# Kernel tuning notes

Hardware: AMD Instinct MI355X
Metric: run time of the kernel (lower is better)

## Reference

```python
import jax, jax.numpy as jnp
import numpy as np

W = H = 64
CONFIGS = [(1, 3), (2, 3), (3, 3)]  # (dilation, kernel_size)
OUT_PER_CFG = 32
IN_CH = 32


def build_mask():
    # One (W+1, H+1) mask per config, broadcast over (out, in) channels.
    masks = []
    for d, k in CONFIGS:
        m = np.zeros((W + 1, H + 1), dtype=np.float32)
        k1 = (k - 1) * (d - 1) + k  # effective dilated kernel extent
        s1 = (W - k1) // 2 + 1
        e1 = (W + k1) // 2 + 1
        s2 = (H - k1) // 2 + 1
        e2 = (H + k1) // 2 + 1
        m[s1:e1:d, s2:e2:d] = 1.0
        masks.append(np.broadcast_to(m, (OUT_PER_CFG, 1, W + 1, H + 1)))
    return jnp.asarray(np.concatenate(masks, axis=0))  # (96, 1, 65, 65)


def setup_inputs() -> dict:
    key = jax.random.key(0)
    k1, k2 = jax.random.split(key)
    x = jax.random.normal(k1, (16, IN_CH, W, H), dtype=jnp.float32)
    # small init so tanh does not saturate
    weight = jax.random.normal(k2, (OUT_PER_CFG * len(CONFIGS), IN_CH, W + 1, H + 1), dtype=jnp.float32) * 0.01
    mask = build_mask()
    gamma = jnp.ones((OUT_PER_CFG * len(CONFIGS),), dtype=jnp.float32)
    beta = jnp.zeros((OUT_PER_CFG * len(CONFIGS),), dtype=jnp.float32)
    return {"x": x, "weight": weight, "mask": mask, "gamma": gamma, "beta": beta}


def reference(x, weight, mask, gamma, beta):
    # circular pad: last dim by H//2 each side, dim -2 by W//2 each side
    xp = jnp.pad(x, ((0, 0), (0, 0), (W // 2, W // 2), (H // 2, H // 2)), mode="wrap")
    y = jax.lax.conv_general_dilated(
        xp, weight * mask,
        window_strides=(1, 1), padding="VALID",
        dimension_numbers=("NCHW", "OIHW", "NCHW"),
    )  # (B, 96, 64, 64)
    # BatchNorm2d in training mode: batch statistics over (N, H, W), eps=1e-5
    mean = jnp.mean(y, axis=(0, 2, 3))
    var = jnp.var(y, axis=(0, 2, 3))
    yn = (y - mean[None, :, None, None]) * jax.lax.rsqrt(var + 1e-5)[None, :, None, None]
    yn = yn * gamma[None, :, None, None] + beta[None, :, None, None]
    return jnp.tanh(yn)
```

## Files before the change

kernel.cpp:

```cpp
#include <hip/hip_runtime.h>
#include <math.h>

#define BATCH 16
#define CIN 32
#define COUT 96
#define WH 64
#define IMG (WH*WH)
#define NPIX (BATCH*IMG)
#define YELEMS (BATCH*COUT*IMG)
#define NPART 256
#define PWELEMS (3*9*32*32)
#define XTELEMS (BATCH*IMG*CIN)

typedef __attribute__((ext_vector_type(8))) short short8;
typedef __attribute__((ext_vector_type(4))) float floatx4;

__device__ __forceinline__ unsigned short f2bf(float f) {
    union { float f; unsigned u; } v; v.f = f;
    unsigned r = v.u + 0x7FFFu + ((v.u >> 16) & 1u);
    return (unsigned short)(r >> 16);
}
__device__ __forceinline__ float bf2f(unsigned short u) {
    union { unsigned u; float f; } v; v.u = (unsigned)u << 16; return v.f;
}

#define GLDS(src, dst) __builtin_amdgcn_global_load_lds( \
    (const __attribute__((address_space(1))) void*)(src), \
    (__attribute__((address_space(3))) void*)(dst), 16, 0, 0)

__device__ __forceinline__ float fast_tanh(float xv) {
    float e = __expf(2.0f * xv);
    return fmaf(-2.0f, __builtin_amdgcn_rcpf(e + 1.0f), 1.0f);
}

__global__ __launch_bounds__(256) void prep_kernel(
    const float* __restrict__ x, const float* __restrict__ w,
    unsigned short* __restrict__ xT, unsigned short* __restrict__ pw)
{
    int blk = blockIdx.x;
    if (blk < 256) {
        int t   = blk * 256 + threadIdx.x;
        int b   = t >> 12;
        int pix = t & 4095;
        const float* xb = x + (size_t)b * CIN * IMG + pix;
        unsigned packed[16];
#pragma unroll
        for (int c2 = 0; c2 < 16; c2++) {
            unsigned short lo = f2bf(xb[(size_t)(2 * c2) * IMG]);
            unsigned short hi = f2bf(xb[(size_t)(2 * c2 + 1) * IMG]);
            packed[c2] = (unsigned)lo | ((unsigned)hi << 16);
        }
        uint4* dst = (uint4*)(xT + (size_t)t * 32);
#pragma unroll
        for (int k = 0; k < 4; k++)
            dst[k] = make_uint4(packed[4 * k], packed[4 * k + 1],
                                packed[4 * k + 2], packed[4 * k + 3]);
    } else {
        int e = (blk - 256) * 256 + threadIdx.x;
        if (e >= PWELEMS) return;
        int cfg = e / (9 * 1024);
        int rem = e % (9 * 1024);
        int tap = rem >> 10;
        int oc  = (rem >> 5) & 31;
        int c   = rem & 31;
        int d   = cfg + 1;
        int du  = tap / 3, dv = tap % 3;
        size_t idx = (((size_t)(cfg * 32 + oc) * CIN + c) * 65 + (32 + (du - 1) * d)) * 65
                     + (32 + (dv - 1) * d);
        pw[e] = f2bf(w[idx]);
    }
}

__global__ __launch_bounds__(256, 3) void conv_stats_kernel(
    const unsigned short* __restrict__ xT, const unsigned short* __restrict__ pw,
    unsigned short* __restrict__ yb, float* __restrict__ psum, float* __restrict__ psq)
{
    int bid  = blockIdx.x;
    int rowg = bid & 15;
    int rest = bid >> 4;
    int cfg  = rest % 3;
    int b    = rest / 3;
    int d    = cfg + 1;
    int i0   = rowg * 4;

    int t    = threadIdx.x;
    int wv   = t >> 6;
    int lane = t & 63;
    int l15  = lane & 15;
    int quad = lane >> 4;

    __shared__ __align__(16) unsigned short tile[10 * 2048];
    __shared__ float red_s[4][32];
    __shared__ float red_q[4][32];

    const unsigned short* xTb = xT + (size_t)b * IMG * 32;
#pragma unroll
    for (int rr = 0; rr < 10; rr++) {
        int gi = (i0 - 3 + rr) & 63;
        GLDS(xTb + (size_t)gi * 2048 + t * 8, &tile[rr * 2048 + t * 8]);
    }

    const unsigned short* pwc = pw + (size_t)cfg * 9 * 32 * 32;
    short8 af[2][9];
#pragma unroll
    for (int h = 0; h < 2; h++)
#pragma unroll
        for (int tap = 0; tap < 9; tap++)
            af[h][tap] = *(const short8*)(pwc + ((tap * 32 + h * 16 + l15) * 32 + quad * 8));

    __syncthreads();

    float ss[2][4], qq[2][4];
#pragma unroll
    for (int h = 0; h < 2; h++)
#pragma unroll
        for (int r = 0; r < 4; r++) { ss[h][r] = 0.f; qq[h][r] = 0.f; }

    int row = i0 + wv;
    size_t ybase = ((size_t)b * COUT + cfg * 32) * IMG + (size_t)row * WH;

#pragma unroll 1
    for (int cg = 0; cg < 4; cg++) {
        floatx4 a0 = {0.f, 0.f, 0.f, 0.f};
        floatx4 a1 = {0.f, 0.f, 0.f, 0.f};
#pragma unroll
        for (int du = 0; du < 3; du++) {
            int rowloc = wv + 3 + (du - 1) * d;
            const unsigned short* rbase = &tile[rowloc * 2048 + quad * 8];
#pragma unroll
            for (int dv = 0; dv < 3; dv++) {
                int col = (cg * 16 + l15 + (dv - 1) * d) & 63;
                short8 bf = *(const short8*)(rbase + col * 32);
                a0 = __builtin_amdgcn_mfma_f32_16x16x32_bf16(af[0][du * 3 + dv], bf, a0, 0, 0, 0);
                a1 = __builtin_amdgcn_mfma_f32_16x16x32_bf16(af[1][du * 3 + dv], bf, a1, 0, 0, 0);
            }
        }
        int colg = cg * 16 + l15;
#pragma unroll
        for (int r = 0; r < 4; r++) {
            float v0 = a0[r], v1 = a1[r];
            int m0 = quad * 4 + r;
            yb[ybase + (size_t)m0 * IMG + colg]        = f2bf(v0);
            yb[ybase + (size_t)(16 + m0) * IMG + colg] = f2bf(v1);
            ss[0][r] += v0; qq[0][r] = fmaf(v0, v0, qq[0][r]);
            ss[1][r] += v1; qq[1][r] = fmaf(v1, v1, qq[1][r]);
        }
    }

#pragma unroll
    for (int h = 0; h < 2; h++)
#pragma unroll
        for (int r = 0; r < 4; r++) {
            float s = ss[h][r], q = qq[h][r];
            for (int m = 1; m < 16; m <<= 1) {
                s += __shfl_xor(s, m, 64);
                q += __shfl_xor(q, m, 64);
            }
            if (l15 == 0) {
                red_s[wv][h * 16 + quad * 4 + r] = s;
                red_q[wv][h * 16 + quad * 4 + r] = q;
            }
        }
    __syncthreads();
    if (t < 32) {
        float S = red_s[0][t] + red_s[1][t] + red_s[2][t] + red_s[3][t];
        psum[(size_t)(cfg * 32 + t) * NPART + b * 16 + rowg] = S;
    } else if (t < 64) {
        int o = t - 32;
        float Q = red_q[0][o] + red_q[1][o] + red_q[2][o] + red_q[3][o];
        psq[(size_t)(cfg * 32 + o) * NPART + b * 16 + rowg] = Q;
    }
}

__global__ __launch_bounds__(256) void bn_tanh_kernel(
    const unsigned short* __restrict__ yb, const float* __restrict__ psum,
    const float* __restrict__ psq, const float* __restrict__ gamma,
    const float* __restrict__ beta, float* __restrict__ out)
{
    __shared__ float part[8];
    __shared__ float sc[2];
    int t  = threadIdx.x;
    int ch = blockIdx.x % COUT;

    float s = psum[(size_t)ch * NPART + t];
    float q = psq[(size_t)ch * NPART + t];
    for (int m = 1; m < 64; m <<= 1) {
        s += __shfl_xor(s, m, 64);
        q += __shfl_xor(q, m, 64);
    }
    if ((t & 63) == 0) { part[t >> 6] = s; part[4 + (t >> 6)] = q; }
    __syncthreads();
    if (t == 0) {
        const float inv_n = 1.0f / (float)NPIX;
        float S = part[0] + part[1] + part[2] + part[3];
        float Q = part[4] + part[5] + part[6] + part[7];
        float mean = S * inv_n;
        float var  = Q * inv_n - mean * mean;
        float a    = gamma[ch] * rsqrtf(var + 1e-5f);
        sc[0] = a;
        sc[1] = beta[ch] - mean * a;
    }
    __syncthreads();

    float a = sc[0], bsh = sc[1];
    size_t base = (size_t)blockIdx.x * IMG;
#pragma unroll
    for (int k = 0; k < 2; k++) {
        size_t off = base + k * 2048 + t * 8;
        uint4 raw = *(const uint4*)(yb + off);
        const unsigned short* u = (const unsigned short*)&raw;
        float4 r0, r1;
        r0.x = fast_tanh(fmaf(bf2f(u[0]), a, bsh));
        r0.y = fast_tanh(fmaf(bf2f(u[1]), a, bsh));
        r0.z = fast_tanh(fmaf(bf2f(u[2]), a, bsh));
        r0.w = fast_tanh(fmaf(bf2f(u[3]), a, bsh));
        r1.x = fast_tanh(fmaf(bf2f(u[4]), a, bsh));
        r1.y = fast_tanh(fmaf(bf2f(u[5]), a, bsh));
        r1.z = fast_tanh(fmaf(bf2f(u[6]), a, bsh));
        r1.w = fast_tanh(fmaf(bf2f(u[7]), a, bsh));
        *(float4*)(out + off)     = r0;
        *(float4*)(out + off + 4) = r1;
    }
}

extern "C" void kernel_launch(void* const* d_in, const int* in_sizes, int n_in,
                              void* d_out, int out_size, void* d_ws, size_t ws_size,
                              hipStream_t stream) {
    const float* x     = (const float*)d_in[0];
    const float* w     = (const float*)d_in[1];
    const float* gamma = (const float*)d_in[3];
    const float* beta  = (const float*)d_in[4];
    float* out = (float*)d_out;

    unsigned short* xT = (unsigned short*)d_ws;
    unsigned short* pw = xT + XTELEMS;
    unsigned short* yb = pw + PWELEMS + 32;
    float* psum = (float*)(yb + YELEMS);
    float* psq  = psum + COUT * NPART;

    prep_kernel<<<256 + (PWELEMS + 255) / 256, 256, 0, stream>>>(x, w, xT, pw);
    conv_stats_kernel<<<768, 256, 0, stream>>>(xT, pw, yb, psum, psq);
    bn_tanh_kernel<<<BATCH * COUT, 256, 0, stream>>>(yb, psum, psq, gamma, beta, out);
}
```

Before: 118.0 us.

## Fuse prep, conv+stats and BN+tanh into one cooperative kernel

Merges the three launches into a single cooperative kernel that uses two grid-wide syncs: one after converting x and the weights to bf16, and one after writing the partial BN statistics. The conv results stay packed in registers, so the bf16 intermediate y never goes to global memory and the separate bn_tanh pass is removed. This saves launch overhead and a round trip of y through memory. In exchange it relies on all 768 blocks being co-resident (3 per CU by launch bounds), adds grid-sync cost, and stores output with 16-wide strided scalar writes instead of vectorised ones. It falls back to the old three-kernel path if the cooperative launch fails.

```diff
diff --git a/kernel.cpp b/kernel.cpp
--- a/kernel.cpp
+++ b/kernel.cpp
@@ -1,4 +1,5 @@
 #include <hip/hip_runtime.h>
+#include <hip/hip_cooperative_groups.h>
 #include <math.h>
 
 #define BATCH 16
@@ -12,6 +13,8 @@
 #define PWELEMS (3*9*32*32)
 #define XTELEMS (BATCH*IMG*CIN)
 
+namespace coopg = cooperative_groups;
+
 typedef __attribute__((ext_vector_type(8))) short short8;
 typedef __attribute__((ext_vector_type(4))) float floatx4;
 
@@ -31,6 +34,194 @@
 __device__ __forceinline__ float fast_tanh(float xv) {
     float e = __expf(2.0f * xv);
     return fmaf(-2.0f, __builtin_amdgcn_rcpf(e + 1.0f), 1.0f);
+}
+
+__global__ __launch_bounds__(256, 3) void fused_kernel(
+    const float* __restrict__ x, const float* __restrict__ w,
+    unsigned short* __restrict__ xT, unsigned short* __restrict__ pw,
+    float* __restrict__ psum, float* __restrict__ psq,
+    const float* __restrict__ gamma, const float* __restrict__ beta,
+    float* __restrict__ out)
+{
+    __shared__ __align__(16) unsigned short tile[10 * 2048];
+    __shared__ float red_s[4][32];
+    __shared__ float red_q[4][32];
+    __shared__ float sc_a[32];
+    __shared__ float sc_b[32];
+
+    int t   = threadIdx.x;
+    int gid = blockIdx.x * 256 + t;
+
+    if (gid < 2 * NPIX) {
+        int pt   = gid >> 1;
+        int half = gid & 1;
+        int b    = pt >> 12;
+        int pix  = pt & 4095;
+        const float* xb = x + ((size_t)b * CIN + half * 16) * IMG + pix;
+        unsigned packed[8];
+#pragma unroll
+        for (int c2 = 0; c2 < 8; c2++) {
+            unsigned short lo = f2bf(xb[(size_t)(2 * c2) * IMG]);
+            unsigned short hi = f2bf(xb[(size_t)(2 * c2 + 1) * IMG]);
+            packed[c2] = (unsigned)lo | ((unsigned)hi << 16);
+        }
+        uint4* dst = (uint4*)(xT + (size_t)pt * 32 + half * 16);
+        dst[0] = make_uint4(packed[0], packed[1], packed[2], packed[3]);
+        dst[1] = make_uint4(packed[4], packed[5], packed[6], packed[7]);
+    } else if (gid < 2 * NPIX + PWELEMS) {
+        int e   = gid - 2 * NPIX;
+        int cfg = e / (9 * 1024);
+        int rem = e % (9 * 1024);
+        int tap = rem >> 10;
+        int oc  = (rem >> 5) & 31;
+        int c   = rem & 31;
+        int dd  = cfg + 1;
+        int du  = tap / 3, dv = tap % 3;
+        size_t idx = (((size_t)(cfg * 32 + oc) * CIN + c) * 65 + (32 + (du - 1) * dd)) * 65
+                     + (32 + (dv - 1) * dd);
+        pw[e] = f2bf(w[idx]);
+    }
+    __threadfence();
+    coopg::this_grid().sync();
+
+    int bid  = blockIdx.x;
+    int rowg = bid & 15;
+    int rest = bid >> 4;
+    int cfg  = rest % 3;
+    int b    = rest / 3;
+    int d    = cfg + 1;
+    int i0   = rowg * 4;
+
+    int wv   = t >> 6;
+    int lane = t & 63;
+    int l15  = lane & 15;
+    int quad = lane >> 4;
+
+    const unsigned short* xTb = xT + (size_t)b * IMG * 32;
+#pragma unroll
+    for (int rr = 0; rr < 10; rr++) {
+        int gi = (i0 - 3 + rr) & 63;
+        GLDS(xTb + (size_t)gi * 2048 + t * 8, &tile[rr * 2048 + t * 8]);
+    }
+
+    const unsigned short* pwc = pw + (size_t)cfg * 9 * 32 * 32;
+    short8 af[2][9];
+#pragma unroll
+    for (int h = 0; h < 2; h++)
+#pragma unroll
+        for (int tap = 0; tap < 9; tap++)
+            af[h][tap] = *(const short8*)(pwc + ((tap * 32 + h * 16 + l15) * 32 + quad * 8));
+
+    __syncthreads();
+
+    float ss[2][4], qq[2][4];
+#pragma unroll
+    for (int h = 0; h < 2; h++)
+#pragma unroll
+        for (int r = 0; r < 4; r++) { ss[h][r] = 0.f; qq[h][r] = 0.f; }
+
+    unsigned ypk[2][4][2];
+    int row = i0 + wv;
+
+#pragma unroll
+    for (int cgi = 0; cgi < 4; cgi++) {
+        floatx4 a0 = {0.f, 0.f, 0.f, 0.f};
+        floatx4 a1 = {0.f, 0.f, 0.f, 0.f};
+#pragma unroll
+        for (int du = 0; du < 3; du++) {
+            int rowloc = wv + 3 + (du - 1) * d;
+            const unsigned short* rbase = &tile[rowloc * 2048 + quad * 8];
+#pragma unroll
+            for (int dv = 0; dv < 3; dv++) {
+                int col = (cgi * 16 + l15 + (dv - 1) * d) & 63;
+                short8 bf = *(const short8*)(rbase + col * 32);
+                a0 = __builtin_amdgcn_mfma_f32_16x16x32_bf16(af[0][du * 3 + dv], bf, a0, 0, 0, 0);
+                a1 = __builtin_amdgcn_mfma_f32_16x16x32_bf16(af[1][du * 3 + dv], bf, a1, 0, 0, 0);
+            }
+        }
+#pragma unroll
+        for (int r = 0; r < 4; r++) {
+            float v0 = a0[r], v1 = a1[r];
+            unsigned short h0 = f2bf(v0), h1 = f2bf(v1);
+            if (cgi & 1) {
+                ypk[0][r][cgi >> 1] |= (unsigned)h0 << 16;
+                ypk[1][r][cgi >> 1] |= (unsigned)h1 << 16;
+            } else {
+                ypk[0][r][cgi >> 1] = (unsigned)h0;
+                ypk[1][r][cgi >> 1] = (unsigned)h1;
+            }
+            ss[0][r] += v0; qq[0][r] = fmaf(v0, v0, qq[0][r]);
+            ss[1][r] += v1; qq[1][r] = fmaf(v1, v1, qq[1][r]);
+        }
+    }
+
+#pragma unroll
+    for (int h = 0; h < 2; h++)
+#pragma unroll
+        for (int r = 0; r < 4; r++) {
+            float s = ss[h][r], q = qq[h][r];
+            for (int m = 1; m < 16; m <<= 1) {
+                s += __shfl_xor(s, m, 64);
+                q += __shfl_xor(q, m, 64);
+            }
+            if (l15 == 0) {
+                red_s[wv][h * 16 + quad * 4 + r] = s;
+                red_q[wv][h * 16 + quad * 4 + r] = q;
+            }
+        }
+    __syncthreads();
+    if (t < 32) {
+        float S = red_s[0][t] + red_s[1][t] + red_s[2][t] + red_s[3][t];
+        psum[(size_t)(cfg * 32 + t) * NPART + b * 16 + rowg] = S;
+    } else if (t < 64) {
+        int o = t - 32;
+        float Q = red_q[0][o] + red_q[1][o] + red_q[2][o] + red_q[3][o];
+        psq[(size_t)(cfg * 32 + o) * NPART + b * 16 + rowg] = Q;
+    }
+    __threadfence();
+    coopg::this_grid().sync();
+
+    {
+        int chl = t >> 3;
+        int seg = t & 7;
+        const float* ps = psum + (size_t)(cfg * 32 + chl) * NPART + seg * 32;
+        const float* pq = psq  + (size_t)(cfg * 32 + chl) * NPART + seg * 32;
+        float S = 0.f, Q = 0.f;
+#pragma unroll
+        for (int k = 0; k < 32; k++) { S += ps[k]; Q += pq[k]; }
+#pragma unroll
+        for (int m = 1; m < 8; m <<= 1) {
+            S += __shfl_xor(S, m, 64);
+            Q += __shfl_xor(Q, m, 64);
+        }
+        if (seg == 0) {
+            const float inv_n = 1.0f / (float)NPIX;
+            float mean = S * inv_n;
+            float var  = Q * inv_n - mean * mean;
+            float a    = gamma[cfg * 32 + chl] * rsqrtf(var + 1e-5f);
+            sc_a[chl] = a;
+            sc_b[chl] = beta[cfg * 32 + chl] - mean * a;
+        }
+    }
+    __syncthreads();
+
+#pragma unroll
+    for (int h = 0; h < 2; h++)
+#pragma unroll
+        for (int r = 0; r < 4; r++) {
+            int m0  = quad * 4 + r;
+            int chl = h * 16 + m0;
+            float a  = sc_a[chl];
+            float bb = sc_b[chl];
+            float* obase = out + ((size_t)b * COUT + cfg * 32 + chl) * IMG
+                               + (size_t)row * WH + l15;
+#pragma unroll
+            for (int g = 0; g < 2; g++) {
+                unsigned pk = ypk[h][r][g];
+                obase[(2 * g) * 16]     = fast_tanh(fmaf(bf2f((unsigned short)(pk & 0xffffu)), a, bb));
+                obase[(2 * g + 1) * 16] = fast_tanh(fmaf(bf2f((unsigned short)(pk >> 16)), a, bb));
+            }
+        }
 }
 
 __global__ __launch_bounds__(256) void prep_kernel(
@@ -238,7 +429,15 @@
     float* psum = (float*)(yb + YELEMS);
     float* psq  = psum + COUT * NPART;
 
-    prep_kernel<<<256 + (PWELEMS + 255) / 256, 256, 0, stream>>>(x, w, xT, pw);
-    conv_stats_kernel<<<768, 256, 0, stream>>>(xT, pw, yb, psum, psq);
-    bn_tanh_kernel<<<BATCH * COUT, 256, 0, stream>>>(yb, psum, psq, gamma, beta, out);
-}
+    void* args[] = {(void*)&x, (void*)&w, (void*)&xT, (void*)&pw,
+                    (void*)&psum, (void*)&psq, (void*)&gamma, (void*)&beta,
+                    (void*)&out};
+    hipError_t err = hipLaunchCooperativeKernel((const void*)fused_kernel,
+                                                dim3(768), dim3(256),
+                                                args, 0, stream);
+    if (err != hipSuccess) {
+        prep_kernel<<<256 + (PWELEMS + 255) / 256, 256, 0, stream>>>(x, w, xT, pw);
+        conv_stats_kernel<<<768, 256, 0, stream>>>(xT, pw, yb, psum, psq);
+        bn_tanh_kernel<<<BATCH * COUT, 256, 0, stream>>>(yb, psum, psq, gamma, beta, out);
+    }
+}
```

After: 416.0 us. +252.4%, slower.

## Fuse conv, batch-norm stats and tanh via grid-wide atomic barrier

Applied to the files above, without the earlier changes.

Merges the conv+stats kernel and the BN+tanh kernel into one persistent-style kernel. Conv outputs stay in registers as packed bf16, channel sums are reduced with global float atomics, and all 768 blocks then spin on a global counter before normalising and writing fp32 output. This removes the bf16 intermediate round trip through memory and one kernel launch. The barrier only works if all 768 blocks are resident at once (3 per CU with 256 CUs), so it risks deadlock otherwise. The atomics also make the reduction order nondeterministic, and the output stores are scattered scalar writes rather than vectorised ones.

```diff
diff --git a/kernel.cpp b/kernel.cpp
--- a/kernel.cpp
+++ b/kernel.cpp
@@ -7,10 +7,9 @@
 #define WH 64
 #define IMG (WH*WH)
 #define NPIX (BATCH*IMG)
-#define YELEMS (BATCH*COUT*IMG)
-#define NPART 256
 #define PWELEMS (3*9*32*32)
 #define XTELEMS (BATCH*IMG*CIN)
+#define NBLK 768
 
 typedef __attribute__((ext_vector_type(8))) short short8;
 typedef __attribute__((ext_vector_type(4))) float floatx4;
@@ -35,7 +34,9 @@
 
 __global__ __launch_bounds__(256) void prep_kernel(
     const float* __restrict__ x, const float* __restrict__ w,
-    unsigned short* __restrict__ xT, unsigned short* __restrict__ pw)
+    unsigned short* __restrict__ xT, unsigned short* __restrict__ pw,
+    float* __restrict__ gsum, float* __restrict__ gsq,
+    unsigned* __restrict__ cnt)
 {
     int blk = blockIdx.x;
     if (blk < 256) {
@@ -55,7 +56,7 @@
         for (int k = 0; k < 4; k++)
             dst[k] = make_uint4(packed[4 * k], packed[4 * k + 1],
                                 packed[4 * k + 2], packed[4 * k + 3]);
-    } else {
+    } else if (blk < 364) {
         int e = (blk - 256) * 256 + threadIdx.x;
         if (e >= PWELEMS) return;
         int cfg = e / (9 * 1024);
@@ -68,13 +69,26 @@
         size_t idx = (((size_t)(cfg * 32 + oc) * CIN + c) * 65 + (32 + (du - 1) * d)) * 65
                      + (32 + (dv - 1) * d);
         pw[e] = f2bf(w[idx]);
-    }
-}
-
-__global__ __launch_bounds__(256, 3) void conv_stats_kernel(
+    } else {
+        int e = threadIdx.x;
+        if (e < COUT) { gsum[e] = 0.f; gsq[e] = 0.f; }
+        if (e == COUT) *cnt = 0u;
+    }
+}
+
+__global__ __launch_bounds__(256, 3) void conv_bn_kernel(
     const unsigned short* __restrict__ xT, const unsigned short* __restrict__ pw,
-    unsigned short* __restrict__ yb, float* __restrict__ psum, float* __restrict__ psq)
+    float* __restrict__ gsum, float* __restrict__ gsq,
+    unsigned* __restrict__ cnt,
+    const float* __restrict__ gamma, const float* __restrict__ beta,
+    float* __restrict__ out)
 {
+    __shared__ __align__(16) unsigned short tile[10 * 2048];
+    __shared__ float red_s[4][32];
+    __shared__ float red_q[4][32];
+    __shared__ float sc_a[32];
+    __shared__ float sc_b[32];
+
     int bid  = blockIdx.x;
     int rowg = bid & 15;
     int rest = bid >> 4;
@@ -89,10 +103,6 @@
     int l15  = lane & 15;
     int quad = lane >> 4;
 
-    __shared__ __align__(16) unsigned short tile[10 * 2048];
-    __shared__ float red_s[4][32];
-    __shared__ float red_q[4][32];
-
     const unsigned short* xTb = xT + (size_t)b * IMG * 32;
 #pragma unroll
     for (int rr = 0; rr < 10; rr++) {
@@ -116,11 +126,11 @@
 #pragma unroll
         for (int r = 0; r < 4; r++) { ss[h][r] = 0.f; qq[h][r] = 0.f; }
 
+    unsigned ypk[2][4][2];
     int row = i0 + wv;
-    size_t ybase = ((size_t)b * COUT + cfg * 32) * IMG + (size_t)row * WH;
-
-#pragma unroll 1
-    for (int cg = 0; cg < 4; cg++) {
+
+#pragma unroll
+    for (int cgi = 0; cgi < 4; cgi++) {
         floatx4 a0 = {0.f, 0.f, 0.f, 0.f};
         floatx4 a1 = {0.f, 0.f, 0.f, 0.f};
 #pragma unroll
@@ -129,19 +139,23 @@
             const unsigned short* rbase = &tile[rowloc * 2048 + quad * 8];
 #pragma unroll
             for (int dv = 0; dv < 3; dv++) {
-                int col = (cg * 16 + l15 + (dv - 1) * d) & 63;
+                int col = (cgi * 16 + l15 + (dv - 1) * d) & 63;
                 short8 bf = *(const short8*)(rbase + col * 32);
                 a0 = __builtin_amdgcn_mfma_f32_16x16x32_bf16(af[0][du * 3 + dv], bf, a0, 0, 0, 0);
                 a1 = __builtin_amdgcn_mfma_f32_16x16x32_bf16(af[1][du * 3 + dv], bf, a1, 0, 0, 0);
             }
         }
-        int colg = cg * 16 + l15;
 #pragma unroll
         for (int r = 0; r < 4; r++) {
             float v0 = a0[r], v1 = a1[r];
-            int m0 = quad * 4 + r;
-            yb[ybase + (size_t)m0 * IMG + colg]        = f2bf(v0);
-            yb[ybase + (size_t)(16 + m0) * IMG + colg] = f2bf(v1);
+            unsigned short h0 = f2bf(v0), h1 = f2bf(v1);
+            if (cgi & 1) {
+                ypk[0][r][cgi >> 1] |= (unsigned)h0 << 16;
+                ypk[1][r][cgi >> 1] |= (unsigned)h1 << 16;
+            } else {
+                ypk[0][r][cgi >> 1] = (unsigned)h0;
+                ypk[1][r][cgi >> 1] = (unsigned)h1;
+            }
             ss[0][r] += v0; qq[0][r] = fmaf(v0, v0, qq[0][r]);
             ss[1][r] += v1; qq[1][r] = fmaf(v1, v1, qq[1][r]);
         }
@@ -162,65 +176,54 @@
             }
         }
     __syncthreads();
+
     if (t < 32) {
         float S = red_s[0][t] + red_s[1][t] + red_s[2][t] + red_s[3][t];
-        psum[(size_t)(cfg * 32 + t) * NPART + b * 16 + rowg] = S;
+        atomicAdd(&gsum[cfg * 32 + t], S);
     } else if (t < 64) {
         int o = t - 32;
         float Q = red_q[0][o] + red_q[1][o] + red_q[2][o] + red_q[3][o];
-        psq[(size_t)(cfg * 32 + o) * NPART + b * 16 + rowg] = Q;
-    }
-}
-
-__global__ __launch_bounds__(256) void bn_tanh_kernel(
-    const unsigned short* __restrict__ yb, const float* __restrict__ psum,
-    const float* __restrict__ psq, const float* __restrict__ gamma,
-    const float* __restrict__ beta, float* __restrict__ out)
-{
-    __shared__ float part[8];
-    __shared__ float sc[2];
-    int t  = threadIdx.x;
-    int ch = blockIdx.x % COUT;
-
-    float s = psum[(size_t)ch * NPART + t];
-    float q = psq[(size_t)ch * NPART + t];
-    for (int m = 1; m < 64; m <<= 1) {
-        s += __shfl_xor(s, m, 64);
-        q += __shfl_xor(q, m, 64);
-    }
-    if ((t & 63) == 0) { part[t >> 6] = s; part[4 + (t >> 6)] = q; }
-    __syncthreads();
+        atomicAdd(&gsq[cfg * 32 + o], Q);
+    }
+    __syncthreads();
+
     if (t == 0) {
+        __hip_atomic_fetch_add(cnt, 1u, __ATOMIC_RELEASE, __HIP_MEMORY_SCOPE_AGENT);
+        while (__hip_atomic_load(cnt, __ATOMIC_RELAXED, __HIP_MEMORY_SCOPE_AGENT) < NBLK)
+            __builtin_amdgcn_s_sleep(8);
+    }
+    __syncthreads();
+
+    if (t < 32) {
+        int ch = cfg * 32 + t;
+        float S = __hip_atomic_load(&gsum[ch], __ATOMIC_RELAXED, __HIP_MEMORY_SCOPE_AGENT);
+        float Q = __hip_atomic_load(&gsq[ch],  __ATOMIC_RELAXED, __HIP_MEMORY_SCOPE_AGENT);
         const float inv_n = 1.0f / (float)NPIX;
-        float S = part[0] + part[1] + part[2] + part[3];
-        float Q = part[4] + part[5] + part[6] + part[7];
         float mean = S * inv_n;
         float var  = Q * inv_n - mean * mean;
         float a    = gamma[ch] * rsqrtf(var + 1e-5f);
-        sc[0] = a;
-        sc[1] = beta[ch] - mean * a;
-    }
-    __syncthreads();
-
-    float a = sc[0], bsh = sc[1];
-    size_t base = (size_t)blockIdx.x * IMG;
-#pragma unroll
-    for (int k = 0; k < 2; k++) {
-        size_t off = base + k * 2048 + t * 8;
-        uint4 raw = *(const uint4*)(yb + off);
-        const unsigned short* u = (const unsigned short*)&raw;
-        float4 r0, r1;
-        r0.x = fast_tanh(fmaf(bf2f(u[0]), a, bsh));
-        r0.y = fast_tanh(fmaf(bf2f(u[1]), a, bsh));
-        r0.z = fast_tanh(fmaf(bf2f(u[2]), a, bsh));
-        r0.w = fast_tanh(fmaf(bf2f(u[3]), a, bsh));
-        r1.x = fast_tanh(fmaf(bf2f(u[4]), a, bsh));
-        r1.y = fast_tanh(fmaf(bf2f(u[5]), a, bsh));
-        r1.z = fast_tanh(fmaf(bf2f(u[6]), a, bsh));
-        r1.w = fast_tanh(fmaf(bf2f(u[7]), a, bsh));
-        *(float4*)(out + off)     = r0;
-        *(float4*)(out + off + 4) = r1;
-    }
+        sc_a[t] = a;
+        sc_b[t] = beta[ch] - mean * a;
+    }
+    __syncthreads();
+
+#pragma unroll
+    for (int h = 0; h < 2; h++)
+#pragma unroll
+        for (int r = 0; r < 4; r++) {
+            int m0  = quad * 4 + r;
+            int chl = h * 16 + m0;
+            float a  = sc_a[chl];
+            float bb = sc_b[chl];
+            float* obase = out + ((size_t)b * COUT + cfg * 32 + chl) * IMG
+                               + (size_t)row * WH + l15;
+#pragma unroll
+            for (int g = 0; g < 2; g++) {
+                unsigned pk = ypk[h][r][g];
+                obase[(2 * g) * 16]     = fast_tanh(fmaf(bf2f((unsigned short)(pk & 0xffffu)), a, bb));
+                obase[(2 * g + 1) * 16] = fast_tanh(fmaf(bf2f((unsigned short)(pk >> 16)), a, bb));
+            }
+        }
 }
 
 extern "C" void kernel_launch(void* const* d_in, const int* in_sizes, int n_in,
@@ -234,11 +237,11 @@
 
     unsigned short* xT = (unsigned short*)d_ws;
     unsigned short* pw = xT + XTELEMS;
-    unsigned short* yb = pw + PWELEMS + 32;
-    float* psum = (float*)(yb + YELEMS);
-    float* psq  = psum + COUT * NPART;
-
-    prep_kernel<<<256 + (PWELEMS + 255) / 256, 256, 0, stream>>>(x, w, xT, pw);
-    conv_stats_kernel<<<768, 256, 0, stream>>>(xT, pw, yb, psum, psq);
-    bn_tanh_kernel<<<BATCH * COUT, 256, 0, stream>>>(yb, psum, psq, gamma, beta, out);
-}
+    float* gsum = (float*)(pw + PWELEMS + 32);
+    float* gsq  = gsum + 128;
+    unsigned* cnt = (unsigned*)(gsq + 128);
+
+    prep_kernel<<<365, 256, 0, stream>>>(x, w, xT, pw, gsum, gsq, cnt);
+    conv_bn_kernel<<<NBLK, 256, 0, stream>>>(xT, pw, gsum, gsq, cnt,
+                                             gamma, beta, out);
+}
```

Measured after the change: 134.9 us. +14.3%, slower.
